# Optimization experiments

Measured on AMD Instinct MI355X. Metric: run time of the kernel, lower is better.

The kernel has to match this reference:

```python
import jax, jax.numpy as jnp
import numpy as np

EMBED = 1024
HEAD = 64

def setup_inputs() -> dict:
    key = jax.random.key(0)
    k1, k2, k3, k4 = jax.random.split(key, 4)
    x = jax.random.normal(k1, (8, 2048, EMBED), dtype=jnp.float32)
    # nn.Linear(E, H, bias=False) weights, stored as [E, H] for x @ W
    W_k = jax.random.normal(k2, (EMBED, HEAD), dtype=jnp.float32) * (EMBED ** -0.5)
    W_q = jax.random.normal(k3, (EMBED, HEAD), dtype=jnp.float32) * (EMBED ** -0.5)
    W_v = jax.random.normal(k4, (EMBED, HEAD), dtype=jnp.float32) * (EMBED ** -0.5)
    return {"x": x, "W_k": W_k, "W_q": W_q, "W_v": W_v}

def reference(x, W_k, W_q, W_v):
    B, T, E = x.shape
    keys = jnp.einsum('bte,eh->bth', x, W_k)
    queries = jnp.einsum('bte,eh->bth', x, W_q)
    values = jnp.einsum('bte,eh->bth', x, W_v)
    # NOTE: original scales by embedding size E, not head size
    scores = jnp.einsum('bqh,bkh->bqk', queries, keys) * (E ** -0.5)
    causal = jnp.tril(jnp.ones((T, T), dtype=bool))
    scores = jnp.where(causal, scores, -jnp.inf)
    weights = jax.nn.softmax(scores, axis=-1)
    return jnp.einsum('bqk,bkh->bqh', weights, values)
```

## Files before the change

kernel.cpp:

```cpp
#include <hip/hip_runtime.h>

typedef __attribute__((ext_vector_type(8))) short bf16x8;
typedef __attribute__((ext_vector_type(4))) float f32x4;
typedef __attribute__((ext_vector_type(4))) unsigned short u16x4;
typedef __attribute__((ext_vector_type(8))) unsigned short u16x8;
typedef __attribute__((ext_vector_type(4))) unsigned int u32x4;

#define MFMA(a, b, c) __builtin_amdgcn_mfma_f32_16x16x32_bf16(a, b, c, 0, 0, 0)

static __device__ __forceinline__ unsigned short f2bf(float x) {
    union { float f; unsigned u; } v; v.f = x;
    unsigned r = v.u + 0x7fffu + ((v.u >> 16) & 1u);
    return (unsigned short)(r >> 16);
}

static __device__ __forceinline__ bf16x8 pack_pa(
    float ea0, float ea1, float ea2, float ea3,
    float eb0, float eb1, float eb2, float eb3, bool odd)
{
    unsigned a1, a2, b1, b2;
    asm("v_cvt_pk_bf16_f32 %0, %1, %2" : "=v"(a1) : "v"(ea0), "v"(ea1));
    asm("v_cvt_pk_bf16_f32 %0, %1, %2" : "=v"(a2) : "v"(ea2), "v"(ea3));
    asm("v_cvt_pk_bf16_f32 %0, %1, %2" : "=v"(b1) : "v"(eb0), "v"(eb1));
    asm("v_cvt_pk_bf16_f32 %0, %1, %2" : "=v"(b2) : "v"(eb2), "v"(eb3));
    asm("v_permlane32_swap_b32 %0, %1" : "+v"(a1), "+v"(b1));
    asm("v_permlane32_swap_b32 %0, %1" : "+v"(a2), "+v"(b2));
    int sa1 = __shfl_xor((int)a1, 16);
    int sa2 = __shfl_xor((int)a2, 16);
    int sb1 = __shfl_xor((int)b1, 16);
    int sb2 = __shfl_xor((int)b2, 16);
    u32x4 paw;
    paw[0] = odd ? (unsigned)sb1 : a1;
    paw[1] = odd ? (unsigned)sb2 : a2;
    paw[2] = odd ? b1 : (unsigned)sa1;
    paw[3] = odd ? b2 : (unsigned)sa2;
    return __builtin_bit_cast(bf16x8, paw);
}

__global__ __launch_bounds__(256) void wtrans_k(
    const float* __restrict__ Wk, const float* __restrict__ Wq,
    const float* __restrict__ Wv, unsigned short* __restrict__ Wt)
{
    __shared__ float tl[64][65];
    const int w = blockIdx.x >> 4, kt = blockIdx.x & 15;
    const float* W = (w == 0) ? Wk : (w == 1) ? Wq : Wv;
    const int tid = threadIdx.x;
#pragma unroll
    for (int rep = 0; rep < 4; rep++) {
        int flat = rep * 256 + tid;
        int rr = flat >> 4, c4 = (flat & 15) * 4;
        f32x4 v = *(const f32x4*)(W + (kt * 64 + rr) * 64 + c4);
#pragma unroll
        for (int jj = 0; jj < 4; jj++) tl[c4 + jj][rr] = v[jj];
    }
    __syncthreads();
#pragma unroll
    for (int rep = 0; rep < 2; rep++) {
        int flat = rep * 256 + tid;
        int n = flat >> 3, k8 = (flat & 7) * 8;
        u16x8 h;
#pragma unroll
        for (int jj = 0; jj < 8; jj++) h[jj] = f2bf(tl[n][k8 + jj]);
        *(u16x8*)(Wt + w * 65536 + n * 1024 + kt * 64 + k8) = h;
    }
}

__global__ __launch_bounds__(512) void qkv_k(
    const float* __restrict__ x, const unsigned short* __restrict__ Wt,
    unsigned short* __restrict__ Qb, unsigned short* __restrict__ Kb,
    unsigned short* __restrict__ Vt)
{
    __shared__ __align__(16) unsigned short xl[2][64][72];
    __shared__ __align__(16) unsigned short wl[2][192][72];
    const int tid = threadIdx.x;
    const int wid = tid >> 6, lane = tid & 63;
    const int lrow = lane & 15, g = lane >> 4;
    const int mbase = blockIdx.x * 64;
    const int msrow = (wid & 3) * 16;
    const int ntbase = (wid >> 2) * 6;

    const int xrow = tid >> 3, xc8 = (tid & 7) * 8;
    const int wrow = tid >> 3, wc8 = (tid & 7) * 8;

    f32x4 acc[6];
#pragma unroll
    for (int j = 0; j < 6; j++) acc[j] = (f32x4){0.f, 0.f, 0.f, 0.f};

    f32x4 vx0, vx1;
    u16x8 rw0, rw1, rw2;
    {
        const float* xs = x + (mbase + xrow) * 1024 + xc8;
        vx0 = *(const f32x4*)(xs);
        vx1 = *(const f32x4*)(xs + 4);
        const unsigned short* ws = Wt + wrow * 1024 + wc8;
        rw0 = *(const u16x8*)(ws);
        rw1 = *(const u16x8*)(ws + 64 * 1024);
        rw2 = *(const u16x8*)(ws + 128 * 1024);
    }

#pragma unroll 1
    for (int t = 0; t < 16; ++t) {
        const int buf = t & 1;
        {
            unsigned d0, d1, d2, d3;
            asm("v_cvt_pk_bf16_f32 %0, %1, %2" : "=v"(d0) : "v"(vx0[0]), "v"(vx0[1]));
            asm("v_cvt_pk_bf16_f32 %0, %1, %2" : "=v"(d1) : "v"(vx0[2]), "v"(vx0[3]));
            asm("v_cvt_pk_bf16_f32 %0, %1, %2" : "=v"(d2) : "v"(vx1[0]), "v"(vx1[1]));
            asm("v_cvt_pk_bf16_f32 %0, %1, %2" : "=v"(d3) : "v"(vx1[2]), "v"(vx1[3]));
            u32x4 pk; pk[0] = d0; pk[1] = d1; pk[2] = d2; pk[3] = d3;
            *(u32x4*)&xl[buf][xrow][xc8] = pk;
            *(u16x8*)&wl[buf][wrow][wc8]       = rw0;
            *(u16x8*)&wl[buf][wrow + 64][wc8]  = rw1;
            *(u16x8*)&wl[buf][wrow + 128][wc8] = rw2;
        }
        if (t < 15) {
            const int kc = (t + 1) * 64;
            const float* xs = x + (mbase + xrow) * 1024 + kc + xc8;
            vx0 = *(const f32x4*)(xs);
            vx1 = *(const f32x4*)(xs + 4);
            const unsigned short* ws = Wt + wrow * 1024 + kc + wc8;
            rw0 = *(const u16x8*)(ws);
            rw1 = *(const u16x8*)(ws + 64 * 1024);
            rw2 = *(const u16x8*)(ws + 128 * 1024);
        }
        __syncthreads();
#pragma unroll
        for (int ks = 0; ks < 2; ks++) {
            bf16x8 a = *(const bf16x8*)&xl[buf][msrow + lrow][ks * 32 + g * 8];
#pragma unroll
            for (int j = 0; j < 6; j++) {
                bf16x8 b = *(const bf16x8*)&wl[buf][(ntbase + j) * 16 + lrow][ks * 32 + g * 8];
                acc[j] = MFMA(a, b, acc[j]);
            }
        }
    }

#pragma unroll
    for (int j = 0; j < 6; j++) {
        int nt = ntbase + j;
        int w = nt >> 2;
        int col = (nt & 3) * 16 + lrow;
        int r0 = mbase + msrow + g * 4;
        if (w == 2) {
            int b = r0 >> 11, tt = r0 & 2047;
            u16x4 pv;
            pv[0] = f2bf(acc[j][0]); pv[1] = f2bf(acc[j][1]);
            pv[2] = f2bf(acc[j][2]); pv[3] = f2bf(acc[j][3]);
            *(u16x4*)(Vt + b * 131072 + col * 2048 + tt) = pv;
        } else {
            unsigned short* dst = (w == 0) ? Kb : Qb;
#pragma unroll
            for (int i = 0; i < 4; i++)
                dst[(r0 + i) * 64 + col] = f2bf(acc[j][i]);
        }
    }
}

__global__ __launch_bounds__(256) void attn_k(
    const unsigned short* __restrict__ Qb, const unsigned short* __restrict__ Kb,
    const unsigned short* __restrict__ Vt, float* __restrict__ pO,
    float* __restrict__ pL)
{
    __shared__ __align__(16) unsigned short klds[2][64][64];
    __shared__ __align__(16) unsigned short vlds[2][64][64];
    const int tid = threadIdx.x;
    const int w = tid >> 6, lane = tid & 63;
    const int lrow = lane & 15, g = lane >> 4;
    const int bid = blockIdx.x;
    const int batch = bid >> 6;
    const int rem = bid & 63;
    const int pi = rem >> 2;
    const int j  = rem & 3;

    const unsigned short* Kbase = Kb + batch * 2048 * 64;
    const unsigned short* Vbase = Vt + batch * 131072;
    const float C2 = 0.03125f * 1.44269504088896f;

    const int sr = tid >> 2;
    const int sc32 = tid & 3;
    const int sb0 = sr * 128 + (((sc32 * 2)     ^ (sr & 7)) << 4);
    const int sb1 = sr * 128 + (((sc32 * 2 + 1) ^ (sr & 7)) << 4);

    const int swz = (lrow & 7) << 4;
    const int rb0 = (lrow) * 128, rb1 = (16 + lrow) * 128,
              rb2 = (32 + lrow) * 128, rb3 = (48 + lrow) * 128;
    const int gk0 = (g << 4) ^ swz;
    const int gk1 = ((4 + g) << 4) ^ swz;
    const bool odd = (g & 1);

#pragma unroll 1
    for (int phase = 0; phase < 2; ++phase) {
        const int B   = phase ? (31 - pi) : pi;
        const int qb  = B * 64;
        const int nch = B + 1;
        const int nc  = (nch > j) ? ((nch - j + 3) >> 2) : 0;

        const unsigned short* Qrow = Qb + (batch * 2048 + qb + w * 16 + lrow) * 64;
        bf16x8 q0 = *(const bf16x8*)(Qrow + g * 8);
        bf16x8 q1 = *(const bf16x8*)(Qrow + 32 + g * 8);
        const int qglob = qb + w * 16 + lrow;

        f32x4 o0 = {0.f,0.f,0.f,0.f}, o1 = o0, o2 = o0, o3 = o0;
        float lsum = 0.f;

        u16x8 rk0 = {}, rk1 = {}, rv0 = {}, rv1 = {};
        if (nc > 0) {
            const int kvb = j * 64;
            const unsigned short* ksrc = Kbase + (kvb + sr) * 64 + sc32 * 16;
            rk0 = *(const u16x8*)(ksrc); rk1 = *(const u16x8*)(ksrc + 8);
            const unsigned short* vsrc = Vbase + sr * 2048 + kvb + sc32 * 16;
            rv0 = *(const u16x8*)(vsrc); rv1 = *(const u16x8*)(vsrc + 8);
            char* kb = (char*)&klds[0][0][0];
            char* vb = (char*)&vlds[0][0][0];
            *(u16x8*)(kb + sb0) = rk0; *(u16x8*)(kb + sb1) = rk1;
            *(u16x8*)(vb + sb0) = rv0; *(u16x8*)(vb + sb1) = rv1;
        }
        __syncthreads();

        for (int idx = 0; idx < nc; ++idx) {
            const int c = j + idx * 4;
            const int cur = idx & 1;
            const int kvbase = c * 64;
            if (idx + 1 < nc) {
                const int kvb = kvbase + 256;
                const unsigned short* ksrc = Kbase + (kvb + sr) * 64 + sc32 * 16;
                rk0 = *(const u16x8*)(ksrc); rk1 = *(const u16x8*)(ksrc + 8);
                const unsigned short* vsrc = Vbase + sr * 2048 + kvb + sc32 * 16;
                rv0 = *(const u16x8*)(vsrc); rv1 = *(const u16x8*)(vsrc + 8);
            }

            const char* kb = (const char*)&klds[cur][0][0];
            const char* vb = (const char*)&vlds[cur][0][0];

            f32x4 t0 = {0.f,0.f,0.f,0.f}, t1 = t0, t2 = t0, t3 = t0;
            {
                bf16x8 a;
                a = *(const bf16x8*)(kb + rb0 + gk0); t0 = MFMA(a, q0, t0);
                a = *(const bf16x8*)(kb + rb0 + gk1); t0 = MFMA(a, q1, t0);
                a = *(const bf16x8*)(kb + rb1 + gk0); t1 = MFMA(a, q0, t1);
                a = *(const bf16x8*)(kb + rb1 + gk1); t1 = MFMA(a, q1, t1);
                a = *(const bf16x8*)(kb + rb2 + gk0); t2 = MFMA(a, q0, t2);
                a = *(const bf16x8*)(kb + rb2 + gk1); t2 = MFMA(a, q1, t2);
                a = *(const bf16x8*)(kb + rb3 + gk0); t3 = MFMA(a, q0, t3);
                a = *(const bf16x8*)(kb + rb3 + gk1); t3 = MFMA(a, q1, t3);
            }

            const bool maskc = (c == nch - 1);
            float eA[4], eB[4], eC[4], eD[4];
#pragma unroll
            for (int u = 0; u < 4; u++) {
                float v0 = t0[u] * C2, v1 = t1[u] * C2,
                      v2 = t2[u] * C2, v3 = t3[u] * C2;
                if (maskc) {
                    int kvr = kvbase + g * 4 + u;
                    v0 = (kvr      > qglob) ? -INFINITY : v0;
                    v1 = (kvr + 16 > qglob) ? -INFINITY : v1;
                    v2 = (kvr + 32 > qglob) ? -INFINITY : v2;
                    v3 = (kvr + 48 > qglob) ? -INFINITY : v3;
                }
                eA[u] = __builtin_exp2f(v0);
                eB[u] = __builtin_exp2f(v1);
                eC[u] = __builtin_exp2f(v2);
                eD[u] = __builtin_exp2f(v3);
                lsum += (eA[u] + eB[u]) + (eC[u] + eD[u]);
            }

            bf16x8 pa0 = pack_pa(eA[0],eA[1],eA[2],eA[3], eB[0],eB[1],eB[2],eB[3], odd);
            bf16x8 pa1 = pack_pa(eC[0],eC[1],eC[2],eC[3], eD[0],eD[1],eD[2],eD[3], odd);

            {
                bf16x8 vv;
                vv = *(const bf16x8*)(vb + rb0 + gk0); o0 = MFMA(pa0, vv, o0);
                vv = *(const bf16x8*)(vb + rb0 + gk1); o0 = MFMA(pa1, vv, o0);
                vv = *(const bf16x8*)(vb + rb1 + gk0); o1 = MFMA(pa0, vv, o1);
                vv = *(const bf16x8*)(vb + rb1 + gk1); o1 = MFMA(pa1, vv, o1);
                vv = *(const bf16x8*)(vb + rb2 + gk0); o2 = MFMA(pa0, vv, o2);
                vv = *(const bf16x8*)(vb + rb2 + gk1); o2 = MFMA(pa1, vv, o2);
                vv = *(const bf16x8*)(vb + rb3 + gk0); o3 = MFMA(pa0, vv, o3);
                vv = *(const bf16x8*)(vb + rb3 + gk1); o3 = MFMA(pa1, vv, o3);
            }

            __syncthreads();
            if (idx + 1 < nc) {
                char* kw = (char*)&klds[cur ^ 1][0][0];
                char* vw = (char*)&vlds[cur ^ 1][0][0];
                *(u16x8*)(kw + sb0) = rk0; *(u16x8*)(kw + sb1) = rk1;
                *(u16x8*)(vw + sb0) = rv0; *(u16x8*)(vw + sb1) = rv1;
            }
            __syncthreads();
        }

        const int qrow0 = batch * 2048 + qb + w * 16;
        float* po = pO + ((size_t)j * 16384 + qrow0) * 64;
#pragma unroll
        for (int u = 0; u < 4; u++) {
            int r = (g * 4 + u) * 64;
            po[r +      lrow] = o0[u];
            po[r + 16 + lrow] = o1[u];
            po[r + 32 + lrow] = o2[u];
            po[r + 48 + lrow] = o3[u];
        }
        lsum += __shfl_xor(lsum, 16);
        lsum += __shfl_xor(lsum, 32);
        if (lane < 16) pL[j * 16384 + qrow0 + lane] = lsum;
        __syncthreads();
    }
}

__global__ __launch_bounds__(256) void comb_k(
    const float* __restrict__ pO, const float* __restrict__ pL,
    float* __restrict__ out)
{
    const int J = 16384 * 64;
    int id = blockIdx.x * 256 + threadIdx.x;
    int row = id >> 2, q = (id & 3) * 16;
    float inv = 1.f / (pL[row] + pL[16384 + row] + pL[32768 + row] + pL[49152 + row]);
    const float* p0 = pO + row * 64 + q;
    float* op = out + row * 64 + q;
#pragma unroll
    for (int k = 0; k < 4; k++) {
        f32x4 s = *(const f32x4*)(p0 + 4 * k)
                + *(const f32x4*)(p0 + J + 4 * k)
                + *(const f32x4*)(p0 + 2 * J + 4 * k)
                + *(const f32x4*)(p0 + 3 * J + 4 * k);
        *(f32x4*)(op + 4 * k) = s * inv;
    }
}

extern "C" void kernel_launch(void* const* d_in, const int* in_sizes, int n_in,
                              void* d_out, int out_size, void* d_ws, size_t ws_size,
                              hipStream_t stream) {
    const float* x  = (const float*)d_in[0];
    const float* Wk = (const float*)d_in[1];
    const float* Wq = (const float*)d_in[2];
    const float* Wv = (const float*)d_in[3];
    float* out = (float*)d_out;

    unsigned short* Wt = (unsigned short*)d_ws;
    unsigned short* Kb = Wt + 3 * 65536;
    unsigned short* Qb = Kb + 16384 * 64;
    unsigned short* Vt = Qb + 16384 * 64;
    float* pO = (float*)(Vt + 131072 * 8);
    float* pL = pO + 4 * 16384 * 64;

    wtrans_k<<<48, 256, 0, stream>>>(Wk, Wq, Wv, Wt);
    qkv_k<<<256, 512, 0, stream>>>(x, Wt, Qb, Kb, Vt);
    attn_k<<<512, 256, 0, stream>>>(Qb, Kb, Vt, pO, pL);
    comb_k<<<256, 256, 0, stream>>>(pO, pL, out);
}
```

Measured before the change: 49.37 us.

## Split QKV blocks to 32 rows and give each attention query band its own block

The QKV projection kernel now uses 256-thread blocks covering 32 rows instead of 512-thread blocks covering 64 rows, which doubles the grid to 512 blocks. The attention kernel drops its two-phase paired-band loop and launches one block per (band, batch, KV split) for 1024 blocks. Bands are ordered heaviest first so the long causal bands start early. The intent is to fill more CUs and balance load through the hardware scheduler rather than manual pairing, at the cost of more W-tile reloads per row in the QKV kernel and more block launch overhead.

Result: no change. 48.42 us (-1.9%).

```diff
diff --git a/kernel.cpp b/kernel.cpp
--- a/kernel.cpp
+++ b/kernel.cpp
@@ -65,37 +65,39 @@
     }
 }
 
-__global__ __launch_bounds__(512) void qkv_k(
+__global__ __launch_bounds__(256) void qkv_k(
     const float* __restrict__ x, const unsigned short* __restrict__ Wt,
     unsigned short* __restrict__ Qb, unsigned short* __restrict__ Kb,
     unsigned short* __restrict__ Vt)
 {
-    __shared__ __align__(16) unsigned short xl[2][64][72];
+    __shared__ __align__(16) unsigned short xl[2][32][72];
     __shared__ __align__(16) unsigned short wl[2][192][72];
     const int tid = threadIdx.x;
     const int wid = tid >> 6, lane = tid & 63;
     const int lrow = lane & 15, g = lane >> 4;
-    const int mbase = blockIdx.x * 64;
-    const int msrow = (wid & 3) * 16;
-    const int ntbase = (wid >> 2) * 6;
-
-    const int xrow = tid >> 3, xc8 = (tid & 7) * 8;
-    const int wrow = tid >> 3, wc8 = (tid & 7) * 8;
+    const int mbase = blockIdx.x * 32;
+    const int msrow = (wid & 1) * 16;
+    const int ntbase = (wid >> 1) * 6;
+
+    const int srow = tid >> 3, c8 = (tid & 7) * 8;
 
     f32x4 acc[6];
 #pragma unroll
     for (int j = 0; j < 6; j++) acc[j] = (f32x4){0.f, 0.f, 0.f, 0.f};
 
     f32x4 vx0, vx1;
-    u16x8 rw0, rw1, rw2;
+    u16x8 rw0, rw1, rw2, rw3, rw4, rw5;
     {
-        const float* xs = x + (mbase + xrow) * 1024 + xc8;
+        const float* xs = x + (mbase + srow) * 1024 + c8;
         vx0 = *(const f32x4*)(xs);
         vx1 = *(const f32x4*)(xs + 4);
-        const unsigned short* ws = Wt + wrow * 1024 + wc8;
+        const unsigned short* ws = Wt + srow * 1024 + c8;
         rw0 = *(const u16x8*)(ws);
-        rw1 = *(const u16x8*)(ws + 64 * 1024);
-        rw2 = *(const u16x8*)(ws + 128 * 1024);
+        rw1 = *(const u16x8*)(ws + 32 * 1024);
+        rw2 = *(const u16x8*)(ws + 64 * 1024);
+        rw3 = *(const u16x8*)(ws + 96 * 1024);
+        rw4 = *(const u16x8*)(ws + 128 * 1024);
+        rw5 = *(const u16x8*)(ws + 160 * 1024);
     }
 
 #pragma unroll 1
@@ -108,20 +110,26 @@
             asm("v_cvt_pk_bf16_f32 %0, %1, %2" : "=v"(d2) : "v"(vx1[0]), "v"(vx1[1]));
             asm("v_cvt_pk_bf16_f32 %0, %1, %2" : "=v"(d3) : "v"(vx1[2]), "v"(vx1[3]));
             u32x4 pk; pk[0] = d0; pk[1] = d1; pk[2] = d2; pk[3] = d3;
-            *(u32x4*)&xl[buf][xrow][xc8] = pk;
-            *(u16x8*)&wl[buf][wrow][wc8]       = rw0;
-            *(u16x8*)&wl[buf][wrow + 64][wc8]  = rw1;
-            *(u16x8*)&wl[buf][wrow + 128][wc8] = rw2;
+            *(u32x4*)&xl[buf][srow][c8] = pk;
+            *(u16x8*)&wl[buf][srow][c8]        = rw0;
+            *(u16x8*)&wl[buf][srow + 32][c8]   = rw1;
+            *(u16x8*)&wl[buf][srow + 64][c8]   = rw2;
+            *(u16x8*)&wl[buf][srow + 96][c8]   = rw3;
+            *(u16x8*)&wl[buf][srow + 128][c8]  = rw4;
+            *(u16x8*)&wl[buf][srow + 160][c8]  = rw5;
         }
         if (t < 15) {
             const int kc = (t + 1) * 64;
-            const float* xs = x + (mbase + xrow) * 1024 + kc + xc8;
+            const float* xs = x + (mbase + srow) * 1024 + kc + c8;
             vx0 = *(const f32x4*)(xs);
             vx1 = *(const f32x4*)(xs + 4);
-            const unsigned short* ws = Wt + wrow * 1024 + kc + wc8;
+            const unsigned short* ws = Wt + srow * 1024 + kc + c8;
             rw0 = *(const u16x8*)(ws);
-            rw1 = *(const u16x8*)(ws + 64 * 1024);
-            rw2 = *(const u16x8*)(ws + 128 * 1024);
+            rw1 = *(const u16x8*)(ws + 32 * 1024);
+            rw2 = *(const u16x8*)(ws + 64 * 1024);
+            rw3 = *(const u16x8*)(ws + 96 * 1024);
+            rw4 = *(const u16x8*)(ws + 128 * 1024);
+            rw5 = *(const u16x8*)(ws + 160 * 1024);
         }
         __syncthreads();
 #pragma unroll
@@ -167,10 +175,14 @@
     const int w = tid >> 6, lane = tid & 63;
     const int lrow = lane & 15, g = lane >> 4;
     const int bid = blockIdx.x;
-    const int batch = bid >> 6;
-    const int rem = bid & 63;
-    const int pi = rem >> 2;
-    const int j  = rem & 3;
+    const int bandIdx = bid >> 5;
+    const int batch = (bid >> 2) & 7;
+    const int j = bid & 3;
+    const int B = (bandIdx < 16) ? (31 - bandIdx) : (bandIdx - 16);
+
+    const int qb  = B * 64;
+    const int nch = B + 1;
+    const int nc  = (nch > j) ? ((nch - j + 3) >> 2) : 0;
 
     const unsigned short* Kbase = Kb + batch * 2048 * 64;
     const unsigned short* Vbase = Vt + batch * 131072;
@@ -188,123 +200,114 @@
     const int gk1 = ((4 + g) << 4) ^ swz;
     const bool odd = (g & 1);
 
-#pragma unroll 1
-    for (int phase = 0; phase < 2; ++phase) {
-        const int B   = phase ? (31 - pi) : pi;
-        const int qb  = B * 64;
-        const int nch = B + 1;
-        const int nc  = (nch > j) ? ((nch - j + 3) >> 2) : 0;
-
-        const unsigned short* Qrow = Qb + (batch * 2048 + qb + w * 16 + lrow) * 64;
-        bf16x8 q0 = *(const bf16x8*)(Qrow + g * 8);
-        bf16x8 q1 = *(const bf16x8*)(Qrow + 32 + g * 8);
-        const int qglob = qb + w * 16 + lrow;
-
-        f32x4 o0 = {0.f,0.f,0.f,0.f}, o1 = o0, o2 = o0, o3 = o0;
-        float lsum = 0.f;
-
-        u16x8 rk0 = {}, rk1 = {}, rv0 = {}, rv1 = {};
-        if (nc > 0) {
-            const int kvb = j * 64;
+    const unsigned short* Qrow = Qb + (batch * 2048 + qb + w * 16 + lrow) * 64;
+    bf16x8 q0 = *(const bf16x8*)(Qrow + g * 8);
+    bf16x8 q1 = *(const bf16x8*)(Qrow + 32 + g * 8);
+    const int qglob = qb + w * 16 + lrow;
+
+    f32x4 o0 = {0.f,0.f,0.f,0.f}, o1 = o0, o2 = o0, o3 = o0;
+    float lsum = 0.f;
+
+    u16x8 rk0 = {}, rk1 = {}, rv0 = {}, rv1 = {};
+    if (nc > 0) {
+        const int kvb = j * 64;
+        const unsigned short* ksrc = Kbase + (kvb + sr) * 64 + sc32 * 16;
+        rk0 = *(const u16x8*)(ksrc); rk1 = *(const u16x8*)(ksrc + 8);
+        const unsigned short* vsrc = Vbase + sr * 2048 + kvb + sc32 * 16;
+        rv0 = *(const u16x8*)(vsrc); rv1 = *(const u16x8*)(vsrc + 8);
+        char* kb = (char*)&klds[0][0][0];
+        char* vb = (char*)&vlds[0][0][0];
+        *(u16x8*)(kb + sb0) = rk0; *(u16x8*)(kb + sb1) = rk1;
+        *(u16x8*)(vb + sb0) = rv0; *(u16x8*)(vb + sb1) = rv1;
+    }
+    __syncthreads();
+
+    for (int idx = 0; idx < nc; ++idx) {
+        const int c = j + idx * 4;
+        const int cur = idx & 1;
+        const int kvbase = c * 64;
+        if (idx + 1 < nc) {
+            const int kvb = kvbase + 256;
             const unsigned short* ksrc = Kbase + (kvb + sr) * 64 + sc32 * 16;
             rk0 = *(const u16x8*)(ksrc); rk1 = *(const u16x8*)(ksrc + 8);
             const unsigned short* vsrc = Vbase + sr * 2048 + kvb + sc32 * 16;
             rv0 = *(const u16x8*)(vsrc); rv1 = *(const u16x8*)(vsrc + 8);
-            char* kb = (char*)&klds[0][0][0];
-            char* vb = (char*)&vlds[0][0][0];
-            *(u16x8*)(kb + sb0) = rk0; *(u16x8*)(kb + sb1) = rk1;
-            *(u16x8*)(vb + sb0) = rv0; *(u16x8*)(vb + sb1) = rv1;
-        }
+        }
+
+        const char* kb = (const char*)&klds[cur][0][0];
+        const char* vb = (const char*)&vlds[cur][0][0];
+
+        f32x4 t0 = {0.f,0.f,0.f,0.f}, t1 = t0, t2 = t0, t3 = t0;
+        {
+            bf16x8 a;
+            a = *(const bf16x8*)(kb + rb0 + gk0); t0 = MFMA(a, q0, t0);
+            a = *(const bf16x8*)(kb + rb0 + gk1); t0 = MFMA(a, q1, t0);
+            a = *(const bf16x8*)(kb + rb1 + gk0); t1 = MFMA(a, q0, t1);
+            a = *(const bf16x8*)(kb + rb1 + gk1); t1 = MFMA(a, q1, t1);
+            a = *(const bf16x8*)(kb + rb2 + gk0); t2 = MFMA(a, q0, t2);
+            a = *(const bf16x8*)(kb + rb2 + gk1); t2 = MFMA(a, q1, t2);
+            a = *(const bf16x8*)(kb + rb3 + gk0); t3 = MFMA(a, q0, t3);
+            a = *(const bf16x8*)(kb + rb3 + gk1); t3 = MFMA(a, q1, t3);
+        }
+
+        const bool maskc = (c == nch - 1);
+        float eA[4], eB[4], eC[4], eD[4];
+#pragma unroll
+        for (int u = 0; u < 4; u++) {
+            float v0 = t0[u] * C2, v1 = t1[u] * C2,
+                  v2 = t2[u] * C2, v3 = t3[u] * C2;
+            if (maskc) {
+                int kvr = kvbase + g * 4 + u;
+                v0 = (kvr      > qglob) ? -INFINITY : v0;
+                v1 = (kvr + 16 > qglob) ? -INFINITY : v1;
+                v2 = (kvr + 32 > qglob) ? -INFINITY : v2;
+                v3 = (kvr + 48 > qglob) ? -INFINITY : v3;
+            }
+            eA[u] = __builtin_exp2f(v0);
+            eB[u] = __builtin_exp2f(v1);
+            eC[u] = __builtin_exp2f(v2);
+            eD[u] = __builtin_exp2f(v3);
+            lsum += (eA[u] + eB[u]) + (eC[u] + eD[u]);
+        }
+
+        bf16x8 pa0 = pack_pa(eA[0],eA[1],eA[2],eA[3], eB[0],eB[1],eB[2],eB[3], odd);
+        bf16x8 pa1 = pack_pa(eC[0],eC[1],eC[2],eC[3], eD[0],eD[1],eD[2],eD[3], odd);
+
+        {
+            bf16x8 vv;
+            vv = *(const bf16x8*)(vb + rb0 + gk0); o0 = MFMA(pa0, vv, o0);
+            vv = *(const bf16x8*)(vb + rb0 + gk1); o0 = MFMA(pa1, vv, o0);
+            vv = *(const bf16x8*)(vb + rb1 + gk0); o1 = MFMA(pa0, vv, o1);
+            vv = *(const bf16x8*)(vb + rb1 + gk1); o1 = MFMA(pa1, vv, o1);
+            vv = *(const bf16x8*)(vb + rb2 + gk0); o2 = MFMA(pa0, vv, o2);
+            vv = *(const bf16x8*)(vb + rb2 + gk1); o2 = MFMA(pa1, vv, o2);
+            vv = *(const bf16x8*)(vb + rb3 + gk0); o3 = MFMA(pa0, vv, o3);
+            vv = *(const bf16x8*)(vb + rb3 + gk1); o3 = MFMA(pa1, vv, o3);
+        }
+
         __syncthreads();
-
-        for (int idx = 0; idx < nc; ++idx) {
-            const int c = j + idx * 4;
-            const int cur = idx & 1;
-            const int kvbase = c * 64;
-            if (idx + 1 < nc) {
-                const int kvb = kvbase + 256;
-                const unsigned short* ksrc = Kbase + (kvb + sr) * 64 + sc32 * 16;
-                rk0 = *(const u16x8*)(ksrc); rk1 = *(const u16x8*)(ksrc + 8);
-                const unsigned short* vsrc = Vbase + sr * 2048 + kvb + sc32 * 16;
-                rv0 = *(const u16x8*)(vsrc); rv1 = *(const u16x8*)(vsrc + 8);
-            }
-
-            const char* kb = (const char*)&klds[cur][0][0];
-            const char* vb = (const char*)&vlds[cur][0][0];
-
-            f32x4 t0 = {0.f,0.f,0.f,0.f}, t1 = t0, t2 = t0, t3 = t0;
-            {
-                bf16x8 a;
-                a = *(const bf16x8*)(kb + rb0 + gk0); t0 = MFMA(a, q0, t0);
-                a = *(const bf16x8*)(kb + rb0 + gk1); t0 = MFMA(a, q1, t0);
-                a = *(const bf16x8*)(kb + rb1 + gk0); t1 = MFMA(a, q0, t1);
-                a = *(const bf16x8*)(kb + rb1 + gk1); t1 = MFMA(a, q1, t1);
-                a = *(const bf16x8*)(kb + rb2 + gk0); t2 = MFMA(a, q0, t2);
-                a = *(const bf16x8*)(kb + rb2 + gk1); t2 = MFMA(a, q1, t2);
-                a = *(const bf16x8*)(kb + rb3 + gk0); t3 = MFMA(a, q0, t3);
-                a = *(const bf16x8*)(kb + rb3 + gk1); t3 = MFMA(a, q1, t3);
-            }
-
-            const bool maskc = (c == nch - 1);
-            float eA[4], eB[4], eC[4], eD[4];
-#pragma unroll
-            for (int u = 0; u < 4; u++) {
-                float v0 = t0[u] * C2, v1 = t1[u] * C2,
-                      v2 = t2[u] * C2, v3 = t3[u] * C2;
-                if (maskc) {
-                    int kvr = kvbase + g * 4 + u;
-                    v0 = (kvr      > qglob) ? -INFINITY : v0;
-                    v1 = (kvr + 16 > qglob) ? -INFINITY : v1;
-                    v2 = (kvr + 32 > qglob) ? -INFINITY : v2;
-                    v3 = (kvr + 48 > qglob) ? -INFINITY : v3;
-                }
-                eA[u] = __builtin_exp2f(v0);
-                eB[u] = __builtin_exp2f(v1);
-                eC[u] = __builtin_exp2f(v2);
-                eD[u] = __builtin_exp2f(v3);
-                lsum += (eA[u] + eB[u]) + (eC[u] + eD[u]);
-            }
-
-            bf16x8 pa0 = pack_pa(eA[0],eA[1],eA[2],eA[3], eB[0],eB[1],eB[2],eB[3], odd);
-            bf16x8 pa1 = pack_pa(eC[0],eC[1],eC[2],eC[3], eD[0],eD[1],eD[2],eD[3], odd);
-
-            {
-                bf16x8 vv;
-                vv = *(const bf16x8*)(vb + rb0 + gk0); o0 = MFMA(pa0, vv, o0);
-                vv = *(const bf16x8*)(vb + rb0 + gk1); o0 = MFMA(pa1, vv, o0);
-                vv = *(const bf16x8*)(vb + rb1 + gk0); o1 = MFMA(pa0, vv, o1);
-                vv = *(const bf16x8*)(vb + rb1 + gk1); o1 = MFMA(pa1, vv, o1);
-                vv = *(const bf16x8*)(vb + rb2 + gk0); o2 = MFMA(pa0, vv, o2);
-                vv = *(const bf16x8*)(vb + rb2 + gk1); o2 = MFMA(pa1, vv, o2);
-                vv = *(const bf16x8*)(vb + rb3 + gk0); o3 = MFMA(pa0, vv, o3);
-                vv = *(const bf16x8*)(vb + rb3 + gk1); o3 = MFMA(pa1, vv, o3);
-            }
-
-            __syncthreads();
-            if (idx + 1 < nc) {
-                char* kw = (char*)&klds[cur ^ 1][0][0];
-                char* vw = (char*)&vlds[cur ^ 1][0][0];
-                *(u16x8*)(kw + sb0) = rk0; *(u16x8*)(kw + sb1) = rk1;
-                *(u16x8*)(vw + sb0) = rv0; *(u16x8*)(vw + sb1) = rv1;
-            }
-            __syncthreads();
-        }
-
-        const int qrow0 = batch * 2048 + qb + w * 16;
-        float* po = pO + ((size_t)j * 16384 + qrow0) * 64;
-#pragma unroll
-        for (int u = 0; u < 4; u++) {
-            int r = (g * 4 + u) * 64;
-            po[r +      lrow] = o0[u];
-            po[r + 16 + lrow] = o1[u];
-            po[r + 32 + lrow] = o2[u];
-            po[r + 48 + lrow] = o3[u];
-        }
-        lsum += __shfl_xor(lsum, 16);
-        lsum += __shfl_xor(lsum, 32);
-        if (lane < 16) pL[j * 16384 + qrow0 + lane] = lsum;
+        if (idx + 1 < nc) {
+            char* kw = (char*)&klds[cur ^ 1][0][0];
+            char* vw = (char*)&vlds[cur ^ 1][0][0];
+            *(u16x8*)(kw + sb0) = rk0; *(u16x8*)(kw + sb1) = rk1;
+            *(u16x8*)(vw + sb0) = rv0; *(u16x8*)(vw + sb1) = rv1;
+        }
         __syncthreads();
     }
+
+    const int qrow0 = batch * 2048 + qb + w * 16;
+    float* po = pO + ((size_t)j * 16384 + qrow0) * 64;
+#pragma unroll
+    for (int u = 0; u < 4; u++) {
+        int r = (g * 4 + u) * 64;
+        po[r +      lrow] = o0[u];
+        po[r + 16 + lrow] = o1[u];
+        po[r + 32 + lrow] = o2[u];
+        po[r + 48 + lrow] = o3[u];
+    }
+    lsum += __shfl_xor(lsum, 16);
+    lsum += __shfl_xor(lsum, 32);
+    if (lane < 16) pL[j * 16384 + qrow0 + lane] = lsum;
 }
 
 __global__ __launch_bounds__(256) void comb_k(
@@ -344,7 +347,7 @@
     float* pL = pO + 4 * 16384 * 64;
 
     wtrans_k<<<48, 256, 0, stream>>>(Wk, Wq, Wv, Wt);
-    qkv_k<<<256, 512, 0, stream>>>(x, Wt, Qb, Kb, Vt);
-    attn_k<<<512, 256, 0, stream>>>(Qb, Kb, Vt, pO, pL);
+    qkv_k<<<512, 256, 0, stream>>>(x, Wt, Qb, Kb, Vt);
+    attn_k<<<1024, 256, 0, stream>>>(Qb, Kb, Vt, pO, pL);
     comb_k<<<256, 256, 0, stream>>>(pO, pL, out);
 }
```
